# Kernel optimization log

Hardware: AMD Instinct MI355X
Metric: run time of the kernel (lower is better)

Reference implementation:

```python
import jax, jax.numpy as jnp
import numpy as np

B, T, I, H = 16, 2048, 512, 512

def setup_inputs() -> dict:
    key = jax.random.key(0)
    k_x, k_wi, k_wr, k_uz = jax.random.split(key, 4)
    inputs = jax.random.normal(k_x, (B, T, I), dtype=jnp.float32)
    W_in = jax.random.normal(k_wi, (H, I), dtype=jnp.float32) / (I ** 0.5)
    b_in = jnp.zeros((H,), dtype=jnp.float32)
    W_rec = jax.random.normal(k_wr, (H, H), dtype=jnp.float32) / (H ** 0.5)
    U_z = jax.random.normal(k_uz, (H, H), dtype=jnp.float32) / (H ** 0.5)
    b_u = jnp.zeros((H,), dtype=jnp.float32)
    return {"inputs": inputs, "W_in": W_in, "b_in": b_in, "W_rec": W_rec, "U_z": U_z, "b_u": b_u}

def reference(inputs, W_in, b_in, W_rec, U_z, b_u):
    # Precompute the input-dependent candidate z for all timesteps in one GEMM:
    # z_t = tanh(x_t @ W_in^T + b_in) has no recurrent dependency.
    z_all = jnp.tanh(jnp.einsum('bti,hi->bth', inputs, W_in) + b_in)  # (B,T,H)
    # Recurrent gated blend must be sequential -> lax.scan over time.
    def step(state, z_t):
        u = jax.nn.sigmoid(state @ W_rec.T + z_t @ U_z.T + b_u)  # (B,H)
        new_state = u * state + (1.0 - u) * z_t
        return new_state, new_state
    init = jnp.zeros((inputs.shape[0], W_rec.shape[0]), dtype=inputs.dtype)
    _, outs = jax.lax.scan(step, init, jnp.swapaxes(z_all, 0, 1))  # scan over T
    return jnp.swapaxes(outs, 0, 1)  # (B,T,H)
```

## Files before the change

### kernel.cpp

```cpp
#include <hip/hip_runtime.h>
#include <cmath>

#define BB 16
#define TT 2048
#define II 512
#define HH 512
#define NSL 4
#define RS  128
#define SCAN_THREADS 512

template<int ACT>
__global__ __launch_bounds__(256) void gemm_nt(const float* __restrict__ A,
                                               const float* __restrict__ B,
                                               const float* __restrict__ bias,
                                               float* __restrict__ C,
                                               int M, int N, int K)
{
    __shared__ float As[16][132];
    __shared__ float Bs[16][132];

    const int m0  = blockIdx.x * 128;
    const int n0  = blockIdx.y * 128;
    const int tid = threadIdx.x;
    const int tm  = tid & 15;
    const int tn  = tid >> 4;

    float acc[8][8];
#pragma unroll
    for (int i = 0; i < 8; ++i)
#pragma unroll
        for (int jj = 0; jj < 8; ++jj) acc[i][jj] = 0.f;

    const int lr = tid >> 1;
    const int lh = (tid & 1) * 8;

    for (int k0 = 0; k0 < K; k0 += 16) {
        const float4* ap = (const float4*)&A[(size_t)(m0 + lr) * K + k0 + lh];
        float4 a0 = ap[0], a1 = ap[1];
        const float4* bp = (const float4*)&B[(size_t)(n0 + lr) * K + k0 + lh];
        float4 b0 = bp[0], b1 = bp[1];

        __syncthreads();
        As[lh + 0][lr] = a0.x; As[lh + 1][lr] = a0.y; As[lh + 2][lr] = a0.z; As[lh + 3][lr] = a0.w;
        As[lh + 4][lr] = a1.x; As[lh + 5][lr] = a1.y; As[lh + 6][lr] = a1.z; As[lh + 7][lr] = a1.w;
        Bs[lh + 0][lr] = b0.x; Bs[lh + 1][lr] = b0.y; Bs[lh + 2][lr] = b0.z; Bs[lh + 3][lr] = b0.w;
        Bs[lh + 4][lr] = b1.x; Bs[lh + 5][lr] = b1.y; Bs[lh + 6][lr] = b1.z; Bs[lh + 7][lr] = b1.w;
        __syncthreads();

#pragma unroll
        for (int kk = 0; kk < 16; ++kk) {
            float4 av0 = *(const float4*)&As[kk][tm * 8];
            float4 av1 = *(const float4*)&As[kk][tm * 8 + 4];
            float4 bv0 = *(const float4*)&Bs[kk][tn * 8];
            float4 bv1 = *(const float4*)&Bs[kk][tn * 8 + 4];
            const float ar[8] = {av0.x, av0.y, av0.z, av0.w, av1.x, av1.y, av1.z, av1.w};
            const float br[8] = {bv0.x, bv0.y, bv0.z, bv0.w, bv1.x, bv1.y, bv1.z, bv1.w};
#pragma unroll
            for (int i = 0; i < 8; ++i)
#pragma unroll
                for (int jj = 0; jj < 8; ++jj)
                    acc[i][jj] = fmaf(ar[i], br[jj], acc[i][jj]);
        }
    }

    float bias_r[8];
#pragma unroll
    for (int jj = 0; jj < 8; ++jj) bias_r[jj] = bias[n0 + tn * 8 + jj];

#pragma unroll
    for (int i = 0; i < 8; ++i) {
        const int m = m0 + tm * 8 + i;
        float o[8];
#pragma unroll
        for (int jj = 0; jj < 8; ++jj) {
            float v = acc[i][jj] + bias_r[jj];
            o[jj] = (ACT == 1) ? tanhf(v) : v;
        }
        float4* cp = (float4*)&C[(size_t)m * N + n0 + tn * 8];
        cp[0] = make_float4(o[0], o[1], o[2], o[3]);
        cp[1] = make_float4(o[4], o[5], o[6], o[7]);
    }
}

__device__ __forceinline__ unsigned long long load_b64_sc0(const unsigned long long* p)
{
    unsigned long long v;
    asm volatile("global_load_dwordx2 %0, %1, off sc0\n\t"
                 "s_waitcnt vmcnt(0)"
                 : "=v"(v) : "v"(p) : "memory");
    return v;
}

__global__ __launch_bounds__(SCAN_THREADS, 2) void scan_kernel(
    const float* __restrict__ W_rec,
    const float* __restrict__ a_all,
    float* __restrict__ zout,
    unsigned long long* __restrict__ htag,
    unsigned int* __restrict__ xtab)
{
    __shared__ float hs[HH];
    __shared__ float zs[RS];
    __shared__ float as_[RS];
    __shared__ float part[NSL][RS];
    __shared__ float hown[RS];
    __shared__ int   fs_sh;

    const int tid = threadIdx.x;
    const int bid = blockIdx.x;
    const int b   = bid & 15;
    const int s   = bid >> 4;
    const int j0  = s * RS;
    const int j   = tid & (RS - 1);
    const int p   = tid >> 7;
    const bool own = (tid >= j0) && (tid < j0 + RS);

    unsigned int myxcc = 0;
    asm volatile("s_getreg_b32 %0, hwreg(20, 0, 32)" : "=s"(myxcc));
    if (tid == 0)
        __hip_atomic_store(&xtab[bid], 0x80000000u | (myxcc & 0xFFFFu),
                           __ATOMIC_RELAXED, __HIP_MEMORY_SCOPE_AGENT);
    if (tid == 0) {
        unsigned int ids[NSL];
        for (int q = 0; q < NSL; ++q) {
            unsigned int e;
            do {
                e = __hip_atomic_load(&xtab[q * BB + b], __ATOMIC_RELAXED,
                                      __HIP_MEMORY_SCOPE_AGENT);
            } while (!(e & 0x80000000u));
            ids[q] = e;
        }
        fs_sh = (ids[0] == ids[1] && ids[1] == ids[2] && ids[2] == ids[3]) ? 1 : 0;
    }

    float w[128];
    {
        const float4* src = (const float4*)&W_rec[(size_t)(j0 + j) * HH + p * 128];
#pragma unroll
        for (int i = 0; i < 32; ++i) {
            float4 v = src[i];
            w[4 * i + 0] = v.x; w[4 * i + 1] = v.y;
            w[4 * i + 2] = v.z; w[4 * i + 3] = v.w;
        }
    }
    if (tid < RS) hown[tid] = 0.f;
    __syncthreads();
    const bool fastpath = (fs_sh != 0);

    const size_t hbase = (size_t)b * HH;

    for (int t = 0; t < TT; ++t) {
        const size_t rowoff = ((size_t)b * TT + t) * HH + j0;
        float zv = 0.f, av = 0.f;
        if (tid < RS) {
            zv = zout[rowoff + tid];
            av = a_all[rowoff + tid];
        }

        if (own) {
            hs[tid] = hown[tid - j0];
        } else {
            const unsigned long long* hp =
                &htag[(size_t)(t & 1) * BB * HH + hbase + tid];
            const unsigned int want = (unsigned int)t;
            unsigned long long v;
            int k = 0;
            for (;;) {
                if (fastpath && k < 4) v = load_b64_sc0(hp);
                else                   v = __hip_atomic_load(hp, __ATOMIC_RELAXED,
                                                             __HIP_MEMORY_SCOPE_AGENT);
                if ((unsigned int)(v >> 32) == want) break;
                if (++k > 2) __builtin_amdgcn_s_sleep(1);
            }
            hs[tid] = __uint_as_float((unsigned int)v);
        }
        if (tid < RS) { zs[tid] = zv; as_[tid] = av; }
        __syncthreads();

        float acc = 0.f;
        {
            const float4* hv4 = (const float4*)&hs[p * 128];
#pragma unroll
            for (int i = 0; i < 32; ++i) {
                float4 hv = hv4[i];
                acc = fmaf(w[4 * i + 0], hv.x, acc);
                acc = fmaf(w[4 * i + 1], hv.y, acc);
                acc = fmaf(w[4 * i + 2], hv.z, acc);
                acc = fmaf(w[4 * i + 3], hv.w, acc);
            }
        }
        part[p][j] = acc;
        __syncthreads();

        if (tid < RS) {
            float v  = part[0][tid] + part[1][tid] + part[2][tid] + part[3][tid]
                     + as_[tid];
            float u  = 1.f / (1.f + expf(-v));
            float hp = hs[j0 + tid];
            float z  = zs[tid];
            float hn = fmaf(u, hp - z, z);
            hown[tid] = hn;
            unsigned long long pack =
                ((unsigned long long)(unsigned int)(t + 1) << 32) |
                (unsigned long long)__float_as_uint(hn);
            __hip_atomic_store(&htag[(size_t)((t + 1) & 1) * BB * HH + hbase + j0 + tid],
                               pack, __ATOMIC_RELAXED, __HIP_MEMORY_SCOPE_AGENT);
            zout[rowoff + tid] = hn;
        }
        __syncthreads();
    }
}

extern "C" void kernel_launch(void* const* d_in, const int* in_sizes, int n_in,
                              void* d_out, int out_size, void* d_ws, size_t ws_size,
                              hipStream_t stream)
{
    const float* X     = (const float*)d_in[0];
    const float* W_in  = (const float*)d_in[1];
    const float* b_in  = (const float*)d_in[2];
    const float* W_rec = (const float*)d_in[3];
    const float* U_z   = (const float*)d_in[4];
    const float* b_u   = (const float*)d_in[5];
    float* out = (float*)d_out;

    float* a_all = (float*)d_ws;
    unsigned long long* htag =
        (unsigned long long*)((char*)d_ws + (size_t)BB * TT * HH * 4);
    unsigned int* xtab =
        (unsigned int*)((char*)htag + (size_t)2 * BB * HH * 8);

    hipMemsetAsync(htag, 0, (size_t)2 * BB * HH * 8 + 64 * 4, stream);

    dim3 blk(256);
    dim3 g1(BB * TT / 128, HH / 128);
    gemm_nt<1><<<g1, blk, 0, stream>>>(X, W_in, b_in, out, BB * TT, HH, II);
    gemm_nt<0><<<g1, blk, 0, stream>>>(out, U_z, b_u, a_all, BB * TT, HH, HH);
    scan_kernel<<<dim3(BB * NSL), dim3(SCAN_THREADS), 0, stream>>>(W_rec, a_all, out, htag, xtab);
}
```

Baseline: 4.540 ms.

## Remap scan blocks to XCC-local groups and prefetch next-step inputs

The scan kernel now ranks all 64 blocks by their XCC id and assigns (batch, slice) roles so that the four slices of a batch tend to share one XCC, which enables the non-coherent sc0 polling fast path more often. The fast path is also validated at runtime over the first timesteps. The next timestep's z and a values are prefetched during the current step instead of loaded on the critical path. Other changes: the dot product is split into four independent accumulators, hprev is kept in a register, __expf replaces expf, and the final __syncthreads becomes an LDS-wait plus raw barrier. The risk is that the sc0 polling path relies on same-XCC cache behaviour, which is not guaranteed by the memory model.

```diff
diff --git a/kernel.cpp b/kernel.cpp
--- a/kernel.cpp
+++ b/kernel.cpp
@@ -99,38 +99,53 @@
     unsigned int* __restrict__ xtab)
 {
     __shared__ float hs[HH];
-    __shared__ float zs[RS];
-    __shared__ float as_[RS];
     __shared__ float part[NSL][RS];
     __shared__ float hown[RS];
-    __shared__ int   fs_sh;
+    __shared__ unsigned int xccs[64];
+    __shared__ unsigned char rk_xcc[64];
+    __shared__ int myrank_sh;
+    __shared__ int fast_ok;
 
     const int tid = threadIdx.x;
     const int bid = blockIdx.x;
-    const int b   = bid & 15;
-    const int s   = bid >> 4;
-    const int j0  = s * RS;
-    const int j   = tid & (RS - 1);
-    const int p   = tid >> 7;
-    const bool own = (tid >= j0) && (tid < j0 + RS);
 
     unsigned int myxcc = 0;
     asm volatile("s_getreg_b32 %0, hwreg(20, 0, 32)" : "=s"(myxcc));
-    if (tid == 0)
-        __hip_atomic_store(&xtab[bid], 0x80000000u | (myxcc & 0xFFFFu),
+    if (tid == 0) {
+        fast_ok = 0;
+        __hip_atomic_store(&xtab[bid], 0x80000000u | (myxcc & 0xFFu),
                            __ATOMIC_RELAXED, __HIP_MEMORY_SCOPE_AGENT);
-    if (tid == 0) {
-        unsigned int ids[NSL];
-        for (int q = 0; q < NSL; ++q) {
-            unsigned int e;
-            do {
-                e = __hip_atomic_load(&xtab[q * BB + b], __ATOMIC_RELAXED,
-                                      __HIP_MEMORY_SCOPE_AGENT);
-            } while (!(e & 0x80000000u));
-            ids[q] = e;
-        }
-        fs_sh = (ids[0] == ids[1] && ids[1] == ids[2] && ids[2] == ids[3]) ? 1 : 0;
-    }
+    }
+    if (tid < 64) {
+        unsigned int e;
+        do {
+            e = __hip_atomic_load(&xtab[tid], __ATOMIC_RELAXED,
+                                  __HIP_MEMORY_SCOPE_AGENT);
+        } while (!(e & 0x80000000u));
+        xccs[tid] = e & 0xFFu;
+    }
+    __syncthreads();
+    if (tid < 64) {
+        const unsigned int key = (xccs[tid] << 6) | (unsigned int)tid;
+        int r = 0;
+        for (int f = 0; f < 64; ++f)
+            r += (((xccs[f] << 6) | (unsigned int)f) < key);
+        rk_xcc[r] = (unsigned char)xccs[tid];
+        if (tid == bid) myrank_sh = r;
+    }
+    __syncthreads();
+    const int rank = myrank_sh;
+    const int b  = rank >> 2;
+    const int s  = rank & 3;
+    const int g4 = (rank >> 2) << 2;
+    const bool grp_local = (rk_xcc[g4] == rk_xcc[g4 + 1] &&
+                            rk_xcc[g4 + 1] == rk_xcc[g4 + 2] &&
+                            rk_xcc[g4 + 2] == rk_xcc[g4 + 3]);
+
+    const int j0 = s * RS;
+    const int j  = tid & (RS - 1);
+    const int p  = tid >> 7;
+    const bool own = (tid >= j0) && (tid < j0 + RS);
 
     float w[128];
     {
@@ -144,17 +159,18 @@
     }
     if (tid < RS) hown[tid] = 0.f;
     __syncthreads();
-    const bool fastpath = (fs_sh != 0);
 
     const size_t hbase = (size_t)b * HH;
+    float hprev = 0.f;
+    float zv = 0.f, av = 0.f;
+    if (tid < RS) {
+        const size_t r0 = ((size_t)b * TT) * HH + j0 + tid;
+        zv = zout[r0];
+        av = a_all[r0];
+    }
 
     for (int t = 0; t < TT; ++t) {
         const size_t rowoff = ((size_t)b * TT + t) * HH + j0;
-        float zv = 0.f, av = 0.f;
-        if (tid < RS) {
-            zv = zout[rowoff + tid];
-            av = a_all[rowoff + tid];
-        }
 
         if (own) {
             hs[tid] = hown[tid - j0];
@@ -162,43 +178,51 @@
             const unsigned long long* hp =
                 &htag[(size_t)(t & 1) * BB * HH + hbase + tid];
             const unsigned int want = (unsigned int)t;
+            const bool try_fast = grp_local && (t < 8 || fast_ok);
             unsigned long long v;
             int k = 0;
             for (;;) {
-                if (fastpath && k < 4) v = load_b64_sc0(hp);
+                if (try_fast && k < 3) v = load_b64_sc0(hp);
                 else                   v = __hip_atomic_load(hp, __ATOMIC_RELAXED,
                                                              __HIP_MEMORY_SCOPE_AGENT);
-                if ((unsigned int)(v >> 32) == want) break;
-                if (++k > 2) __builtin_amdgcn_s_sleep(1);
+                if ((unsigned int)(v >> 32) == want) {
+                    if (try_fast && k < 3 && t >= 1 && t < 8) fast_ok = 1;
+                    break;
+                }
+                if (++k > 8) __builtin_amdgcn_s_sleep(1);
             }
             hs[tid] = __uint_as_float((unsigned int)v);
         }
-        if (tid < RS) { zs[tid] = zv; as_[tid] = av; }
-        __syncthreads();
-
-        float acc = 0.f;
+        __syncthreads();
+
+        float zv_n = 0.f, av_n = 0.f;
+        if (tid < RS && t + 1 < TT) {
+            zv_n = zout[rowoff + HH + tid];
+            av_n = a_all[rowoff + HH + tid];
+        }
+
+        float ax = 0.f, ay = 0.f, az = 0.f, aw = 0.f;
         {
             const float4* hv4 = (const float4*)&hs[p * 128];
 #pragma unroll
             for (int i = 0; i < 32; ++i) {
                 float4 hv = hv4[i];
-                acc = fmaf(w[4 * i + 0], hv.x, acc);
-                acc = fmaf(w[4 * i + 1], hv.y, acc);
-                acc = fmaf(w[4 * i + 2], hv.z, acc);
-                acc = fmaf(w[4 * i + 3], hv.w, acc);
+                ax = fmaf(w[4 * i + 0], hv.x, ax);
+                ay = fmaf(w[4 * i + 1], hv.y, ay);
+                az = fmaf(w[4 * i + 2], hv.z, az);
+                aw = fmaf(w[4 * i + 3], hv.w, aw);
             }
         }
-        part[p][j] = acc;
+        part[p][j] = (ax + ay) + (az + aw);
         __syncthreads();
 
         if (tid < RS) {
             float v  = part[0][tid] + part[1][tid] + part[2][tid] + part[3][tid]
-                     + as_[tid];
-            float u  = 1.f / (1.f + expf(-v));
-            float hp = hs[j0 + tid];
-            float z  = zs[tid];
-            float hn = fmaf(u, hp - z, z);
+                     + av;
+            float u  = 1.f / (1.f + __expf(-v));
+            float hn = fmaf(u, hprev - zv, zv);
             hown[tid] = hn;
+            hprev = hn;
             unsigned long long pack =
                 ((unsigned long long)(unsigned int)(t + 1) << 32) |
                 (unsigned long long)__float_as_uint(hn);
@@ -206,7 +230,9 @@
                                pack, __ATOMIC_RELAXED, __HIP_MEMORY_SCOPE_AGENT);
             zout[rowoff + tid] = hn;
         }
-        __syncthreads();
+        asm volatile("s_waitcnt lgkmcnt(0)" ::: "memory");
+        __builtin_amdgcn_s_barrier();
+        zv = zv_n; av = av_n;
     }
 }
 
```

Result: slower. 4.711 ms (+3.8%).
